# Kernel optimization log

Hardware: AMD Instinct MI355X
Metric: run time of the kernel (lower is better)

Reference implementation:

```python
import jax, jax.numpy as jnp
import numpy as np

B = 4
P0, P1, P2 = 196608, 49152, 12288
DEG = 8
K = 4
EPS = 1e-5


def _cheb_conv(x, cols, vals, W, b):
    """Chebyshev graph conv. x: (B,P,Cin); cols/vals: (P,DEG) fixed-degree sparse L;
    W: (K*Cin, Cout); b: (Cout,). Recursion: T0=x, T1=Lx, Tk=2 L T_{k-1} - T_{k-2}."""
    def lmul(y):  # sparse matvec per batch/channel: (B,P,C) -> (B,P,C)
        return jnp.einsum('pd,bpdc->bpc', vals, y[:, cols, :])
    t0 = x
    t1 = lmul(t0)
    terms = [t0, t1]
    for _ in range(K - 2):
        t2 = 2.0 * lmul(t1) - t0
        terms.append(t2)
        t0, t1 = t1, t2
    xk = jnp.concatenate(terms, axis=-1)  # (B,P,K*Cin)
    return xk @ W + b


def _layernorm(h, g, bt):
    mu = jnp.mean(h, axis=-1, keepdims=True)
    var = jnp.mean(jnp.square(h - mu), axis=-1, keepdims=True)
    return g * (h - mu) / jnp.sqrt(var + EPS) + bt


def _avg_pool4(h):  # HEALPix nested-order average pooling: (B,P,C) -> (B,P//4,C)
    Bh, P, C = h.shape
    return h.reshape(Bh, P // 4, 4, C).mean(axis=2)


def setup_inputs() -> dict:
    key = jax.random.key(0)
    ks = jax.random.split(key, 16)
    cin, c1, c2, c3 = 16, 64, 128, 256
    hid, emb = 512, 256

    def glorot(k, shape):
        fan_in = shape[0]
        return jax.random.normal(k, shape, jnp.float32) / np.sqrt(fan_in)

    inp = {
        'x': jax.random.normal(ks[0], (B, P0, cin), jnp.float32),
        'cols1': jax.random.randint(ks[1], (P0, DEG), 0, P0),
        'vals1': 0.2 * jax.random.normal(ks[2], (P0, DEG), jnp.float32),
        'cols2': jax.random.randint(ks[3], (P1, DEG), 0, P1),
        'vals2': 0.2 * jax.random.normal(ks[4], (P1, DEG), jnp.float32),
        'cols3': jax.random.randint(ks[5], (P2, DEG), 0, P2),
        'vals3': 0.2 * jax.random.normal(ks[6], (P2, DEG), jnp.float32),
        'W1': glorot(ks[7], (K * cin, c1)), 'b1': jnp.zeros((c1,), jnp.float32),
        'g1': jnp.ones((c1,), jnp.float32), 'bt1': jnp.zeros((c1,), jnp.float32),
        'W2': glorot(ks[8], (K * c1, c2)), 'b2': jnp.zeros((c2,), jnp.float32),
        'g2': jnp.ones((c2,), jnp.float32), 'bt2': jnp.zeros((c2,), jnp.float32),
        'W3': glorot(ks[9], (K * c2, c3)), 'b3': jnp.zeros((c3,), jnp.float32),
        'g3': jnp.ones((c3,), jnp.float32), 'bt3': jnp.zeros((c3,), jnp.float32),
        'mW1': glorot(ks[10], (c3, hid)), 'mb1': jnp.zeros((hid,), jnp.float32),
        'mW2': glorot(ks[11], (hid, emb)), 'mb2': jnp.zeros((emb,), jnp.float32),
    }
    return inp


def reference(x, cols1, vals1, cols2, vals2, cols3, vals3,
              W1, b1, g1, bt1, W2, b2, g2, bt2, W3, b3, g3, bt3,
              mW1, mb1, mW2, mb2):
    # Stage 1: ChebConv -> LayerNorm -> ReLU -> avg pool (4:1)
    h = _cheb_conv(x, cols1, vals1, W1, b1)
    h = jax.nn.relu(_layernorm(h, g1, bt1))
    h = _avg_pool4(h)
    # Stage 2
    h = _cheb_conv(h, cols2, vals2, W2, b2)
    h = jax.nn.relu(_layernorm(h, g2, bt2))
    h = _avg_pool4(h)
    # Stage 3 (last stage: no pooling)
    h = _cheb_conv(h, cols3, vals3, W3, b3)
    h = jax.nn.relu(_layernorm(h, g3, bt3))
    # Global mean pool over pixels, then MLP head (Linear-ReLU-Linear)
    z = h.mean(axis=1)                     # (B, 256)
    z = jax.nn.relu(z @ mW1 + mb1)
    z = z @ mW2 + mb2                      # (B, 256)
    return z
```

## Files before the change

### kernel.cpp

```cpp
#include <hip/hip_runtime.h>
#include <hip/hip_bf16.h>

namespace {

constexpr int B  = 4;
constexpr int P0 = 196608, P1 = 49152, P2 = 12288;
constexpr int DEG = 8;
constexpr float EPS = 1e-5f;
constexpr int NBLK3 = (P2 * B) / 64;
constexpr int RSL = 16;
constexpr int RPB = NBLK3 / RSL;

typedef __attribute__((ext_vector_type(4))) float f32x4;
typedef __attribute__((ext_vector_type(8))) short s16x8;

__device__ __forceinline__ float b2f(unsigned short u) {
    union { unsigned int i; float f; } c; c.i = (unsigned int)u << 16; return c.f;
}
__device__ __forceinline__ unsigned short f2b(float f) {
    __hip_bfloat16 h = __float2bfloat16(f);
    return *reinterpret_cast<unsigned short*>(&h);
}

__device__ __forceinline__ float chebw(const float* __restrict__ W,
                                       int k, int n, int N, int Cin) {
    int t = k / Cin, c = k - t * Cin;
    float v = W[(size_t)k * N + n];
    if (t == 0)      v = v - W[(size_t)(2 * Cin + c) * N + n];
    else if (t == 1) v = v - 3.f * W[(size_t)(3 * Cin + c) * N + n];
    else if (t == 2) v = 2.f * v;
    else             v = 4.f * v;
    return v;
}

__global__ __launch_bounds__(256)
void x2p_kernel(const float* __restrict__ in, unsigned short* __restrict__ out)
{
    long idx = (long)blockIdx.x * blockDim.x + threadIdx.x;
    if (idx >= (long)P0 * B * 2) return;
    int  h = (int)(idx & 1);
    int  b = (int)((idx >> 1) & 3);
    long p = idx >> 3;
    const float* src = in + ((size_t)b * P0 + p) * 16 + h * 8;
    float4 v0 = *(const float4*)src;
    float4 v1 = *(const float4*)(src + 4);
    union { uint4 u; unsigned short s[8]; } o;
    o.s[0] = f2b(v0.x); o.s[1] = f2b(v0.y); o.s[2] = f2b(v0.z); o.s[3] = f2b(v0.w);
    o.s[4] = f2b(v1.x); o.s[5] = f2b(v1.y); o.s[6] = f2b(v1.z); o.s[7] = f2b(v1.w);
    *(uint4*)&out[((size_t)p * B + b) * 16 + h * 8] = o.u;
}

__global__ __launch_bounds__(256)
void wt_all_kernel(const float* __restrict__ W1, const float* __restrict__ W2,
                   const float* __restrict__ W3,
                   const float* __restrict__ mW1, const float* __restrict__ mW2,
                   unsigned short* __restrict__ Wt1, unsigned short* __restrict__ Wt2,
                   unsigned short* __restrict__ Wt3,
                   float* __restrict__ mW1t, float* __restrict__ mW2t)
{
    int i = blockIdx.x * 256 + threadIdx.x;
    if (i < 4096) {
        int n = i % 64, k = i / 64;
        Wt1[n * 64 + k] = f2b(chebw(W1, k, n, 64, 16));
    } else if (i < 36864) {
        int j = i - 4096;
        int n = j % 128, k = j / 128;
        Wt2[n * 256 + k] = f2b(chebw(W2, k, n, 128, 64));
    } else if (i < 167936) {
        int j = i - 36864;
        int n = j % 256, k = j / 256;
        Wt3[n * 512 + k] = f2b(chebw(W3, k, n, 256, 128));
    } else if (i < 299008) {
        int j = i - 167936;
        int n = j % 512, k = j / 512;
        mW1t[(size_t)n * 256 + k] = mW1[j];
    } else if (i < 430080) {
        int j = i - 299008;
        int n = j % 256, k = j / 256;
        mW2t[(size_t)n * 512 + k] = mW2[j];
    }
}

template <int CV8>
__global__ __launch_bounds__(256)
void lmul_v3_kernel(const unsigned short* __restrict__ in,
                    const int* __restrict__ cols, const float* __restrict__ vals,
                    unsigned short* __restrict__ out)
{
    constexpr int ROWS = 256 / CV8;
    __shared__ int   cs[ROWS * DEG];
    __shared__ float vs[ROWS * DEG];
    const int tid = threadIdx.x;
    const long r0 = (long)blockIdx.x * ROWS;
    if (tid < ROWS * DEG) {
        cs[tid] = cols[r0 * DEG + tid];
        vs[tid] = vals[r0 * DEG + tid];
    }
    __syncthreads();

    const int v  = tid & (CV8 - 1);
    const int lr = tid / CV8;
    const uint4* in16 = (const uint4*)in;

    float acc[8] = {0.f,0.f,0.f,0.f,0.f,0.f,0.f,0.f};
#pragma unroll
    for (int d = 0; d < DEG; ++d) {
        int   col = cs[lr * DEG + d];
        float w   = vs[lr * DEG + d];
        union { uint4 u; unsigned short s[8]; } x;
        x.u = in16[(size_t)col * CV8 + v];
#pragma unroll
        for (int j = 0; j < 8; ++j) acc[j] = fmaf(w, b2f(x.s[j]), acc[j]);
    }
    union { uint4 u; unsigned short s[8]; } ou;
#pragma unroll
    for (int j = 0; j < 8; ++j) ou.s[j] = f2b(acc[j]);
    ((uint4*)out)[(size_t)(r0 + lr) * CV8 + v] = ou.u;
}

__global__ __launch_bounds__(256)
void s1_mm_kernel(const unsigned short* __restrict__ t0,
                  const unsigned short* __restrict__ t1,
                  const unsigned short* __restrict__ t2,
                  const unsigned short* __restrict__ t3,
                  const unsigned short* __restrict__ Wt,
                  const float* __restrict__ bias,
                  const float* __restrict__ gam,
                  const float* __restrict__ bet,
                  unsigned short* __restrict__ out)
{
    const int wave = threadIdx.x >> 6;
    const int lane = threadIdx.x & 63;
    const int g    = lane >> 4;
    const int c16  = lane & 15;

    s16x8 wf[2][4];
#pragma unroll
    for (int ks = 0; ks < 2; ++ks)
#pragma unroll
        for (int n = 0; n < 4; ++n)
            wf[ks][n] = *(const s16x8*)&Wt[(size_t)(n * 16 + c16) * 64 + ks * 32 + g * 8];

    float bz[4], gz[4], tz[4];
#pragma unroll
    for (int n = 0; n < 4; ++n) {
        bz[n] = bias[n * 16 + c16];
        gz[n] = gam [n * 16 + c16];
        tz[n] = bet [n * 16 + c16];
    }

    const unsigned short* tb[4] = { t0, t1, t2, t3 };
    const int term0  = g >> 1;
    const int coloff = (g & 1) * 8;
    const int bb     = c16 >> 2;
    const int px     = c16 & 3;

    constexpr int NT = P0 / 4;
    const int wg     = blockIdx.x * 4 + wave;
    const int wstep  = gridDim.x * 4;

    for (int t = wg; t < NT; t += wstep) {
        size_t rowbase = ((size_t)(t * 4 + px) * 4 + bb) * 16 + coloff;
        s16x8 a0 = *(const s16x8*)&tb[term0    ][rowbase];
        s16x8 a1 = *(const s16x8*)&tb[term0 + 2][rowbase];

        f32x4 acc[4];
#pragma unroll
        for (int n = 0; n < 4; ++n) acc[n] = (f32x4){bz[n], bz[n], bz[n], bz[n]};
#pragma unroll
        for (int n = 0; n < 4; ++n)
            acc[n] = __builtin_amdgcn_mfma_f32_16x16x32_bf16(a0, wf[0][n], acc[n], 0, 0, 0);
#pragma unroll
        for (int n = 0; n < 4; ++n)
            acc[n] = __builtin_amdgcn_mfma_f32_16x16x32_bf16(a1, wf[1][n], acc[n], 0, 0, 0);

        float s[4] = {0,0,0,0}, q[4] = {0,0,0,0};
#pragma unroll
        for (int n = 0; n < 4; ++n)
#pragma unroll
            for (int r = 0; r < 4; ++r) {
                float v = acc[n][r];
                s[r] += v; q[r] += v * v;
            }
#pragma unroll
        for (int msk = 1; msk < 16; msk <<= 1)
#pragma unroll
            for (int r = 0; r < 4; ++r) {
                s[r] += __shfl_xor(s[r], msk, 64);
                q[r] += __shfl_xor(q[r], msk, 64);
            }
        float mu[4], rs[4];
#pragma unroll
        for (int r = 0; r < 4; ++r) {
            mu[r] = s[r] * (1.f / 64.f);
            float var = q[r] * (1.f / 64.f) - mu[r] * mu[r];
            rs[r] = rsqrtf(var + EPS);
        }
        size_t ro = ((size_t)t * 4 + g) * 64;
#pragma unroll
        for (int n = 0; n < 4; ++n) {
            float pv = 0.f;
#pragma unroll
            for (int r = 0; r < 4; ++r) {
                float h = fmaf(gz[n] * rs[r], acc[n][r] - mu[r], tz[n]);
                pv += fmaxf(h, 0.f);
            }
            out[ro + n * 16 + c16] = f2b(pv * 0.25f);
        }
    }
}

template <int CIN, int COUT, int GM, int GN, int POOL, int LOG2CIN>
__global__ __launch_bounds__(512)
void cheb_mm_v4_kernel(const unsigned short* __restrict__ t0,
                       const unsigned short* __restrict__ t1,
                       const unsigned short* __restrict__ t2,
                       const unsigned short* __restrict__ t3,
                       const unsigned short* __restrict__ Wt,
                       const float* __restrict__ bias,
                       const float* __restrict__ gam,
                       const float* __restrict__ bet,
                       void* __restrict__ outv)
{
    constexpr int KC   = 4 * CIN;
    constexpr int BM   = GM * 64;
    constexpr int NKCH = KC / 64;
    constexpr int AITS = BM * 8 / 512;
    constexpr int WITS = COUT * 8 / 512;

    __shared__ unsigned short As[BM * 64];
    __shared__ unsigned short Ws[COUT * 64];
    __shared__ float sq[BM][GN][2];

    const int tid  = threadIdx.x;
    const int wv   = tid >> 6;
    const int gm   = wv / GN;
    const int gn   = wv % GN;
    const int lane = tid & 63;
    const int g    = lane >> 4;
    const int c16  = lane & 15;

    const unsigned short* tb[4] = { t0, t1, t2, t3 };

    float bz[4], gz[4], tz[4];
#pragma unroll
    for (int n = 0; n < 4; ++n) {
        int col = gn * 64 + n * 16 + c16;
        bz[n] = bias[col]; gz[n] = gam[col]; tz[n] = bet[col];
    }

    f32x4 acc[4][4];
#pragma unroll
    for (int m = 0; m < 4; ++m)
#pragma unroll
        for (int n = 0; n < 4; ++n)
            acc[m][n] = (f32x4){bz[n], bz[n], bz[n], bz[n]};

    uint4 ra[AITS], rw[WITS];

    auto load_chunk = [&](int kc) {
#pragma unroll
        for (int it = 0; it < AITS; ++it) {
            int i = tid + it * 512;
            int row = i >> 3, v = i & 7;
            int k = kc * 64 + v * 8;
            int term = k >> LOG2CIN;
            int c = k & (CIN - 1);
            size_t srow;
            if constexpr (POOL == 4) {
                int pix = blockIdx.x * (BM / 4) + ((row >> 4) << 2) + (row & 3);
                int rb  = (row >> 2) & 3;
                srow = ((size_t)pix * B + rb) * CIN + c;
            } else {
                srow = ((size_t)(blockIdx.x * BM + row)) * CIN + c;
            }
            ra[it] = *(const uint4*)&tb[term][srow];
        }
#pragma unroll
        for (int it = 0; it < WITS; ++it) {
            int i = tid + it * 512;
            int co = i >> 3, v = i & 7;
            rw[it] = *(const uint4*)&Wt[(size_t)co * KC + kc * 64 + v * 8];
        }
    };
    auto write_chunk = [&]() {
#pragma unroll
        for (int it = 0; it < AITS; ++it) {
            int i = tid + it * 512;
            int row = i >> 3, v = i & 7;
            *(uint4*)((char*)As + row * 128 + ((v * 16) ^ ((row & 7) << 4))) = ra[it];
        }
#pragma unroll
        for (int it = 0; it < WITS; ++it) {
            int i = tid + it * 512;
            int co = i >> 3, v = i & 7;
            *(uint4*)((char*)Ws + co * 128 + ((v * 16) ^ ((co & 7) << 4))) = rw[it];
        }
    };

    load_chunk(0);
    for (int kc = 0; kc < NKCH; ++kc) {
        __syncthreads();
        write_chunk();
        __syncthreads();
        if (kc + 1 < NKCH) load_chunk(kc + 1);
#pragma unroll
        for (int ks = 0; ks < 2; ++ks) {
            const int cb  = ks * 64 + g * 16;
            const int swz = cb ^ ((c16 & 7) << 4);
            s16x8 a[4], bw[4];
#pragma unroll
            for (int m = 0; m < 4; ++m)
                a[m] = *(const s16x8*)((const char*)As + (gm * 64 + m * 16 + c16) * 128 + swz);
#pragma unroll
            for (int n = 0; n < 4; ++n)
                bw[n] = *(const s16x8*)((const char*)Ws + (gn * 64 + n * 16 + c16) * 128 + swz);
#pragma unroll
            for (int n = 0; n < 4; ++n)
#pragma unroll
                for (int m = 0; m < 4; ++m)
                    acc[m][n] = __builtin_amdgcn_mfma_f32_16x16x32_bf16(a[m], bw[n], acc[m][n], 0, 0, 0);
        }
    }

    float sm[4][4], qm[4][4];
#pragma unroll
    for (int m = 0; m < 4; ++m)
#pragma unroll
        for (int r = 0; r < 4; ++r) { sm[m][r] = 0.f; qm[m][r] = 0.f; }
#pragma unroll
    for (int m = 0; m < 4; ++m)
#pragma unroll
        for (int n = 0; n < 4; ++n)
#pragma unroll
            for (int r = 0; r < 4; ++r) {
                float v = acc[m][n][r];
                sm[m][r] += v; qm[m][r] += v * v;
            }
#pragma unroll
    for (int msk = 1; msk < 16; msk <<= 1)
#pragma unroll
        for (int m = 0; m < 4; ++m)
#pragma unroll
            for (int r = 0; r < 4; ++r) {
                sm[m][r] += __shfl_xor(sm[m][r], msk, 64);
                qm[m][r] += __shfl_xor(qm[m][r], msk, 64);
            }
    __syncthreads();
    if (c16 == 0) {
#pragma unroll
        for (int m = 0; m < 4; ++m)
#pragma unroll
            for (int r = 0; r < 4; ++r) {
                sq[gm * 64 + m * 16 + g * 4 + r][gn][0] = sm[m][r];
                sq[gm * 64 + m * 16 + g * 4 + r][gn][1] = qm[m][r];
            }
    }
    __syncthreads();
    float mu[4][4], rs[4][4];
#pragma unroll
    for (int m = 0; m < 4; ++m)
#pragma unroll
        for (int r = 0; r < 4; ++r) {
            int row = gm * 64 + m * 16 + g * 4 + r;
            float ss = 0.f, qq = 0.f;
#pragma unroll
            for (int j = 0; j < GN; ++j) { ss += sq[row][j][0]; qq += sq[row][j][1]; }
            mu[m][r] = ss * (1.f / COUT);
            float var = qq * (1.f / COUT) - mu[m][r] * mu[m][r];
            rs[m][r] = rsqrtf(var + EPS);
        }

    if constexpr (POOL == 4) {
        unsigned short* outp = (unsigned short*)outv;
#pragma unroll
        for (int m = 0; m < 4; ++m) {
            size_t ro = ((size_t)(blockIdx.x * (BM / 16) + gm * 4 + m) * B + g) * COUT + gn * 64;
#pragma unroll
            for (int n = 0; n < 4; ++n) {
                float pv = 0.f;
#pragma unroll
                for (int r = 0; r < 4; ++r) {
                    float h = fmaf(gz[n] * rs[m][r], acc[m][n][r] - mu[m][r], tz[n]);
                    pv += fmaxf(h, 0.f);
                }
                outp[ro + n * 16 + c16] = f2b(pv * 0.25f);
            }
        }
    } else {
        float part[4][4];
#pragma unroll
        for (int n = 0; n < 4; ++n)
#pragma unroll
            for (int r = 0; r < 4; ++r) part[n][r] = 0.f;
#pragma unroll
        for (int m = 0; m < 4; ++m)
#pragma unroll
            for (int n = 0; n < 4; ++n)
#pragma unroll
                for (int r = 0; r < 4; ++r) {
                    float h = fmaf(gz[n] * rs[m][r], acc[m][n][r] - mu[m][r], tz[n]);
                    part[n][r] += fmaxf(h, 0.f);
                }
#pragma unroll
        for (int n = 0; n < 4; ++n)
#pragma unroll
            for (int r = 0; r < 4; ++r) {
                part[n][r] += __shfl_xor(part[n][r], 16, 64);
                part[n][r] += __shfl_xor(part[n][r], 32, 64);
            }
        if (g == 0) {
            float* zb = (float*)outv + ((size_t)(blockIdx.x * GM + gm)) * (B * COUT);
#pragma unroll
            for (int n = 0; n < 4; ++n)
#pragma unroll
                for (int r = 0; r < 4; ++r)
                    zb[(size_t)r * COUT + gn * 64 + n * 16 + c16] = part[n][r];
        }
    }
}

__global__ __launch_bounds__(256)
void zred_kernel(const float* __restrict__ zblk, float* __restrict__ zp2)
{
    int s   = blockIdx.x >> 2;
    int col = (blockIdx.x & 3) * 256 + threadIdx.x;
    float acc = 0.f;
#pragma unroll 8
    for (int r = 0; r < RPB; ++r)
        acc += zblk[(size_t)(s * RPB + r) * (B * 256) + col];
    zp2[(size_t)s * (B * 256) + col] = acc;
}

__global__ __launch_bounds__(256)
void headA_kernel(const float* __restrict__ zp2, const float* __restrict__ mW1t,
                  const float* __restrict__ mb1, float* __restrict__ hh)
{
    __shared__ float zs[B * 256];
    __shared__ float ph[256];
    const int tid = threadIdx.x;
    for (int idx = tid; idx < B * 256; idx += 256) {
        float s = 0.f;
#pragma unroll
        for (int sl = 0; sl < RSL; ++sl) s += zp2[(size_t)sl * (B * 256) + idx];
        zs[idx] = s * (1.f / P2);
    }
    __syncthreads();
    const int jl = tid & 31, b = (tid >> 5) & 3, ig = tid >> 7;
    const int j  = blockIdx.x * 32 + jl;
    const float4* wrow = (const float4*)&mW1t[(size_t)j * 256 + ig * 128];
    const float*  zb   = &zs[b * 256 + ig * 128];
    float acc = 0.f;
#pragma unroll
    for (int i4 = 0; i4 < 32; ++i4) {
        float4 wv = wrow[i4];
        acc += zb[i4*4]*wv.x + zb[i4*4+1]*wv.y + zb[i4*4+2]*wv.z + zb[i4*4+3]*wv.w;
    }
    ph[tid] = acc;
    __syncthreads();
    if (tid < 128) {
        float a = ph[tid] + ph[tid + 128] + mb1[j];
        hh[b * 512 + j] = fmaxf(a, 0.f);
    }
}

__global__ __launch_bounds__(256)
void headB_kernel(const float* __restrict__ hh, const float* __restrict__ mW2t,
                  const float* __restrict__ mb2, float* __restrict__ out)
{
    __shared__ float hs[B * 512];
    __shared__ float ph[256];
    const int tid = threadIdx.x;
    for (int idx = tid; idx < B * 512; idx += 256) hs[idx] = hh[idx];
    __syncthreads();
    const int cl = tid & 31, b = (tid >> 5) & 3, ig = tid >> 7;
    const int c  = blockIdx.x * 32 + cl;
    const float4* wrow = (const float4*)&mW2t[(size_t)c * 512 + ig * 256];
    const float*  hb   = &hs[b * 512 + ig * 256];
    float acc = 0.f;
#pragma unroll
    for (int j4 = 0; j4 < 64; ++j4) {
        float4 wv = wrow[j4];
        acc += hb[j4*4]*wv.x + hb[j4*4+1]*wv.y + hb[j4*4+2]*wv.z + hb[j4*4+3]*wv.w;
    }
    ph[tid] = acc;
    __syncthreads();
    if (tid < 128)
        out[b * 256 + c] = ph[tid] + ph[tid + 128] + mb2[c];
}

}

extern "C" void kernel_launch(void* const* d_in, const int* in_sizes, int n_in,
                              void* d_out, int out_size, void* d_ws, size_t ws_size,
                              hipStream_t stream)
{
    const float* x     = (const float*)d_in[0];
    const int*   cols1 = (const int*)  d_in[1];
    const float* vals1 = (const float*)d_in[2];
    const int*   cols2 = (const int*)  d_in[3];
    const float* vals2 = (const float*)d_in[4];
    const int*   cols3 = (const int*)  d_in[5];
    const float* vals3 = (const float*)d_in[6];
    const float* W1  = (const float*)d_in[7];
    const float* b1  = (const float*)d_in[8];
    const float* g1  = (const float*)d_in[9];
    const float* bt1 = (const float*)d_in[10];
    const float* W2  = (const float*)d_in[11];
    const float* b2  = (const float*)d_in[12];
    const float* g2  = (const float*)d_in[13];
    const float* bt2 = (const float*)d_in[14];
    const float* W3  = (const float*)d_in[15];
    const float* b3  = (const float*)d_in[16];
    const float* g3  = (const float*)d_in[17];
    const float* bt3 = (const float*)d_in[18];
    const float* mW1 = (const float*)d_in[19];
    const float* mb1 = (const float*)d_in[20];
    const float* mW2 = (const float*)d_in[21];
    const float* mb2 = (const float*)d_in[22];
    float* out = (float*)d_out;

    char* w = (char*)d_ws;
    size_t off = 0;
    auto alloc = [&](size_t bytes) -> void* {
        void* p = w + off;
        off += (bytes + 255) & ~(size_t)255;
        return p;
    };
    const size_t E1 = (size_t)B * P0 * 16;
    unsigned short* xb  = (unsigned short*)alloc(E1 * 2);
    unsigned short* t_a = (unsigned short*)alloc(E1 * 2);
    unsigned short* t_b = (unsigned short*)alloc(E1 * 2);
    unsigned short* t_c = (unsigned short*)alloc(E1 * 2);
    unsigned short* h1  = (unsigned short*)alloc((size_t)P1 * B * 64 * 2);
    unsigned short* h2  = (unsigned short*)alloc((size_t)P2 * B * 128 * 2);
    unsigned short* Wt1 = (unsigned short*)alloc(64 * 64 * 2);
    unsigned short* Wt2 = (unsigned short*)alloc(256 * 128 * 2);
    unsigned short* Wt3 = (unsigned short*)alloc(512 * 256 * 2);
    float*          mW1t = (float*)alloc((size_t)512 * 256 * 4);
    float*          mW2t = (float*)alloc((size_t)256 * 512 * 4);
    float*          zblk = (float*)alloc((size_t)NBLK3 * B * 256 * 4);
    float*          zp2  = (float*)alloc((size_t)RSL * B * 256 * 4);
    float*          hh   = (float*)alloc((size_t)B * 512 * 4);

    x2p_kernel<<<(int)(((long)P0 * B * 2 + 255) / 256), 256, 0, stream>>>(x, xb);
    wt_all_kernel<<<(430080 + 255) / 256, 256, 0, stream>>>(
        W1, W2, W3, mW1, mW2, Wt1, Wt2, Wt3, mW1t, mW2t);

    {
        lmul_v3_kernel<8><<<P0 / 32, 256, 0, stream>>>(xb,  cols1, vals1, t_a);
        lmul_v3_kernel<8><<<P0 / 32, 256, 0, stream>>>(t_a, cols1, vals1, t_b);
        lmul_v3_kernel<8><<<P0 / 32, 256, 0, stream>>>(t_b, cols1, vals1, t_c);
        s1_mm_kernel<<<2048, 256, 0, stream>>>(xb, t_a, t_b, t_c, Wt1, b1, g1, bt1, h1);
    }
    {
        lmul_v3_kernel<32><<<P1 / 8, 256, 0, stream>>>(h1,  cols2, vals2, t_a);
        lmul_v3_kernel<32><<<P1 / 8, 256, 0, stream>>>(t_a, cols2, vals2, t_b);
        lmul_v3_kernel<32><<<P1 / 8, 256, 0, stream>>>(t_b, cols2, vals2, t_c);
        cheb_mm_v4_kernel<64, 128, 4, 2, 4, 6><<<(P1 * B) / 256, 512, 0, stream>>>(
            h1, t_a, t_b, t_c, Wt2, b2, g2, bt2, h2);
    }
    {
        lmul_v3_kernel<64><<<P2 / 4, 256, 0, stream>>>(h2,  cols3, vals3, t_a);
        lmul_v3_kernel<64><<<P2 / 4, 256, 0, stream>>>(t_a, cols3, vals3, t_b);
        lmul_v3_kernel<64><<<P2 / 4, 256, 0, stream>>>(t_b, cols3, vals3, t_c);
        cheb_mm_v4_kernel<128, 256, 2, 4, 1, 7><<<(P2 * B) / 128, 512, 0, stream>>>(
            h2, t_a, t_b, t_c, Wt3, b3, g3, bt3, zblk);
    }
    zred_kernel<<<RSL * 4, 256, 0, stream>>>(zblk, zp2);
    headA_kernel<<<16, 256, 0, stream>>>(zp2, mW1t, mb1, hh);
    headB_kernel<<<8, 256, 0, stream>>>(hh, mW2t, mb2, out);

    (void)in_sizes; (void)n_in; (void)out_size; (void)ws_size;
}
```

Measured before the change: 450.5 us.

## Permute output channels for vector stores, drop register prefetch, shrink MM tiles

Reorders the transposed weight rows so each lane owns four consecutive output channels, which turns the scalar bf16/fp32 epilogue stores into ushort4/float4 stores. The register-staged prefetch of the next K chunk in the cheb matmul is replaced by direct global-to-LDS copies, with occupancy hints added through launch bounds. Stage-2 moves to smaller 256-thread blocks and the stage-1 grid is doubled. The aim is fewer registers and more resident waves, at the cost of no longer overlapping the global loads with the MFMA work.

```diff
diff --git a/kernel.cpp b/kernel.cpp
--- a/kernel.cpp
+++ b/kernel.cpp
@@ -31,6 +31,10 @@
     else if (t == 2) v = 2.f * v;
     else             v = 4.f * v;
     return v;
+}
+
+__device__ __forceinline__ int coutmap(int r) {
+    return (r & ~63) + ((r & 15) << 2) + ((r >> 4) & 3);
 }
 
 __global__ __launch_bounds__(256)
@@ -60,16 +64,16 @@
 {
     int i = blockIdx.x * 256 + threadIdx.x;
     if (i < 4096) {
-        int n = i % 64, k = i / 64;
-        Wt1[n * 64 + k] = f2b(chebw(W1, k, n, 64, 16));
+        int r = i / 64, k = i % 64;
+        Wt1[r * 64 + k] = f2b(chebw(W1, k, coutmap(r), 64, 16));
     } else if (i < 36864) {
         int j = i - 4096;
-        int n = j % 128, k = j / 128;
-        Wt2[n * 256 + k] = f2b(chebw(W2, k, n, 128, 64));
+        int r = j / 256, k = j % 256;
+        Wt2[r * 256 + k] = f2b(chebw(W2, k, coutmap(r), 128, 64));
     } else if (i < 167936) {
         int j = i - 36864;
-        int n = j % 256, k = j / 256;
-        Wt3[n * 512 + k] = f2b(chebw(W3, k, n, 256, 128));
+        int r = j / 512, k = j % 512;
+        Wt3[r * 512 + k] = f2b(chebw(W3, k, coutmap(r), 256, 128));
     } else if (i < 299008) {
         int j = i - 167936;
         int n = j % 512, k = j / 512;
@@ -118,7 +122,7 @@
     ((uint4*)out)[(size_t)(r0 + lr) * CV8 + v] = ou.u;
 }
 
-__global__ __launch_bounds__(256)
+__global__ __launch_bounds__(256, 8)
 void s1_mm_kernel(const unsigned short* __restrict__ t0,
                   const unsigned short* __restrict__ t1,
                   const unsigned short* __restrict__ t2,
@@ -144,9 +148,8 @@
     float bz[4], gz[4], tz[4];
 #pragma unroll
     for (int n = 0; n < 4; ++n) {
-        bz[n] = bias[n * 16 + c16];
-        gz[n] = gam [n * 16 + c16];
-        tz[n] = bet [n * 16 + c16];
+        int co = c16 * 4 + n;
+        bz[n] = bias[co]; gz[n] = gam[co]; tz[n] = bet[co];
     }
 
     const unsigned short* tb[4] = { t0, t1, t2, t3 };
@@ -197,6 +200,8 @@
             rs[r] = rsqrtf(var + EPS);
         }
         size_t ro = ((size_t)t * 4 + g) * 64;
+        ushort4 ov;
+        unsigned short* ovp = (unsigned short*)&ov;
 #pragma unroll
         for (int n = 0; n < 4; ++n) {
             float pv = 0.f;
@@ -205,14 +210,15 @@
                 float h = fmaf(gz[n] * rs[r], acc[n][r] - mu[r], tz[n]);
                 pv += fmaxf(h, 0.f);
             }
-            out[ro + n * 16 + c16] = f2b(pv * 0.25f);
-        }
-    }
-}
-
-template <int CIN, int COUT, int GM, int GN, int POOL, int LOG2CIN>
-__global__ __launch_bounds__(512)
-void cheb_mm_v4_kernel(const unsigned short* __restrict__ t0,
+            ovp[n] = f2b(pv * 0.25f);
+        }
+        *(ushort4*)&out[ro + c16 * 4] = ov;
+    }
+}
+
+template <int CIN, int COUT, int GM, int GN, int POOL, int LOG2CIN, int TH, int MINW>
+__global__ __launch_bounds__(TH, MINW)
+void cheb_mm_v7_kernel(const unsigned short* __restrict__ t0,
                        const unsigned short* __restrict__ t1,
                        const unsigned short* __restrict__ t2,
                        const unsigned short* __restrict__ t3,
@@ -225,8 +231,6 @@
     constexpr int KC   = 4 * CIN;
     constexpr int BM   = GM * 64;
     constexpr int NKCH = KC / 64;
-    constexpr int AITS = BM * 8 / 512;
-    constexpr int WITS = COUT * 8 / 512;
 
     __shared__ unsigned short As[BM * 64];
     __shared__ unsigned short Ws[COUT * 64];
@@ -245,7 +249,7 @@
     float bz[4], gz[4], tz[4];
 #pragma unroll
     for (int n = 0; n < 4; ++n) {
-        int col = gn * 64 + n * 16 + c16;
+        int col = gn * 64 + c16 * 4 + n;
         bz[n] = bias[col]; gz[n] = gam[col]; tz[n] = bet[col];
     }
 
@@ -256,12 +260,11 @@
         for (int n = 0; n < 4; ++n)
             acc[m][n] = (f32x4){bz[n], bz[n], bz[n], bz[n]};
 
-    uint4 ra[AITS], rw[WITS];
-
-    auto load_chunk = [&](int kc) {
-#pragma unroll
-        for (int it = 0; it < AITS; ++it) {
-            int i = tid + it * 512;
+    for (int kc = 0; kc < NKCH; ++kc) {
+        if (kc) __syncthreads();
+#pragma unroll
+        for (int it = 0; it < BM * 8 / TH; ++it) {
+            int i = tid + it * TH;
             int row = i >> 3, v = i & 7;
             int k = kc * 64 + v * 8;
             int term = k >> LOG2CIN;
@@ -274,40 +277,20 @@
             } else {
                 srow = ((size_t)(blockIdx.x * BM + row)) * CIN + c;
             }
-            ra[it] = *(const uint4*)&tb[term][srow];
-        }
-#pragma unroll
-        for (int it = 0; it < WITS; ++it) {
-            int i = tid + it * 512;
+            *(uint4*)((char*)As + row * 128 + ((v * 16) ^ ((row & 7) << 4))) =
+                *(const uint4*)&tb[term][srow];
+        }
+#pragma unroll
+        for (int it = 0; it < COUT * 8 / TH; ++it) {
+            int i = tid + it * TH;
             int co = i >> 3, v = i & 7;
-            rw[it] = *(const uint4*)&Wt[(size_t)co * KC + kc * 64 + v * 8];
-        }
-    };
-    auto write_chunk = [&]() {
-#pragma unroll
-        for (int it = 0; it < AITS; ++it) {
-            int i = tid + it * 512;
-            int row = i >> 3, v = i & 7;
-            *(uint4*)((char*)As + row * 128 + ((v * 16) ^ ((row & 7) << 4))) = ra[it];
-        }
-#pragma unroll
-        for (int it = 0; it < WITS; ++it) {
-            int i = tid + it * 512;
-            int co = i >> 3, v = i & 7;
-            *(uint4*)((char*)Ws + co * 128 + ((v * 16) ^ ((co & 7) << 4))) = rw[it];
-        }
-    };
-
-    load_chunk(0);
-    for (int kc = 0; kc < NKCH; ++kc) {
+            *(uint4*)((char*)Ws + co * 128 + ((v * 16) ^ ((co & 7) << 4))) =
+                *(const uint4*)&Wt[(size_t)co * KC + kc * 64 + v * 8];
+        }
         __syncthreads();
-        write_chunk();
-        __syncthreads();
-        if (kc + 1 < NKCH) load_chunk(kc + 1);
 #pragma unroll
         for (int ks = 0; ks < 2; ++ks) {
-            const int cb  = ks * 64 + g * 16;
-            const int swz = cb ^ ((c16 & 7) << 4);
+            const int swz = (ks * 64 + g * 16) ^ ((c16 & 7) << 4);
             s16x8 a[4], bw[4];
 #pragma unroll
             for (int m = 0; m < 4; ++m)
@@ -375,7 +358,10 @@
         unsigned short* outp = (unsigned short*)outv;
 #pragma unroll
         for (int m = 0; m < 4; ++m) {
-            size_t ro = ((size_t)(blockIdx.x * (BM / 16) + gm * 4 + m) * B + g) * COUT + gn * 64;
+            size_t ro = ((size_t)(blockIdx.x * (BM / 16) + gm * 4 + m) * B + g) * COUT
+                        + gn * 64 + c16 * 4;
+            ushort4 ov;
+            unsigned short* ovp = (unsigned short*)&ov;
 #pragma unroll
             for (int n = 0; n < 4; ++n) {
                 float pv = 0.f;
@@ -384,8 +370,9 @@
                     float h = fmaf(gz[n] * rs[m][r], acc[m][n][r] - mu[m][r], tz[n]);
                     pv += fmaxf(h, 0.f);
                 }
-                outp[ro + n * 16 + c16] = f2b(pv * 0.25f);
-            }
+                ovp[n] = f2b(pv * 0.25f);
+            }
+            *(ushort4*)&outp[ro] = ov;
         }
     } else {
         float part[4][4];
@@ -412,10 +399,10 @@
         if (g == 0) {
             float* zb = (float*)outv + ((size_t)(blockIdx.x * GM + gm)) * (B * COUT);
 #pragma unroll
-            for (int n = 0; n < 4; ++n)
-#pragma unroll
-                for (int r = 0; r < 4; ++r)
-                    zb[(size_t)r * COUT + gn * 64 + n * 16 + c16] = part[n][r];
+            for (int r = 0; r < 4; ++r) {
+                float4 fv = make_float4(part[0][r], part[1][r], part[2][r], part[3][r]);
+                *(float4*)&zb[(size_t)r * COUT + gn * 64 + c16 * 4] = fv;
+            }
         }
     }
 }
@@ -551,20 +538,20 @@
         lmul_v3_kernel<8><<<P0 / 32, 256, 0, stream>>>(xb,  cols1, vals1, t_a);
         lmul_v3_kernel<8><<<P0 / 32, 256, 0, stream>>>(t_a, cols1, vals1, t_b);
         lmul_v3_kernel<8><<<P0 / 32, 256, 0, stream>>>(t_b, cols1, vals1, t_c);
-        s1_mm_kernel<<<2048, 256, 0, stream>>>(xb, t_a, t_b, t_c, Wt1, b1, g1, bt1, h1);
+        s1_mm_kernel<<<4096, 256, 0, stream>>>(xb, t_a, t_b, t_c, Wt1, b1, g1, bt1, h1);
     }
     {
         lmul_v3_kernel<32><<<P1 / 8, 256, 0, stream>>>(h1,  cols2, vals2, t_a);
         lmul_v3_kernel<32><<<P1 / 8, 256, 0, stream>>>(t_a, cols2, vals2, t_b);
         lmul_v3_kernel<32><<<P1 / 8, 256, 0, stream>>>(t_b, cols2, vals2, t_c);
-        cheb_mm_v4_kernel<64, 128, 4, 2, 4, 6><<<(P1 * B) / 256, 512, 0, stream>>>(
+        cheb_mm_v7_kernel<64, 128, 2, 2, 4, 6, 256, 4><<<(P1 * B) / 128, 256, 0, stream>>>(
             h1, t_a, t_b, t_c, Wt2, b2, g2, bt2, h2);
     }
     {
         lmul_v3_kernel<64><<<P2 / 4, 256, 0, stream>>>(h2,  cols3, vals3, t_a);
         lmul_v3_kernel<64><<<P2 / 4, 256, 0, stream>>>(t_a, cols3, vals3, t_b);
         lmul_v3_kernel<64><<<P2 / 4, 256, 0, stream>>>(t_b, cols3, vals3, t_c);
-        cheb_mm_v4_kernel<128, 256, 2, 4, 1, 7><<<(P2 * B) / 128, 512, 0, stream>>>(
+        cheb_mm_v7_kernel<128, 256, 2, 4, 1, 7, 512, 4><<<(P2 * B) / 128, 512, 0, stream>>>(
             h2, t_a, t_b, t_c, Wt3, b3, g3, bt3, zblk);
     }
     zred_kernel<<<RSL * 4, 256, 0, stream>>>(zblk, zp2);
```

After: 467.8 us. +3.8%, slower.
